# Performance work log

Hardware: AMD Instinct MI355X
Metric: run time of the kernel (lower is better)

Reference implementation:

```python
import jax, jax.numpy as jnp
import numpy as np

N_NODES = 100000
N_EDGES = 1600000
IN_F, OUT_F = 25, 50


def setup_inputs() -> dict:
    key = jax.random.key(0)
    k1, k2, k3, k4 = jax.random.split(key, 4)
    x = jax.random.normal(k1, (N_NODES, IN_F), dtype=jnp.float32)
    W = jax.random.normal(k2, (IN_F, OUT_F), dtype=jnp.float32) * (1.0 / np.sqrt(IN_F))
    b = jax.random.normal(k3, (OUT_F,), dtype=jnp.float32) * 0.01
    edge_index = jax.random.randint(k4, (2, N_EDGES), 0, N_NODES, dtype=jnp.int64)
    return {"x": x, "W": W, "b": b, "edge_index": edge_index}


def reference(x, W, b, edge_index):
    # GCNConv(normalize=False): linear transform, then add-aggregate over edges, + bias.
    src, dst = edge_index[0], edge_index[1]
    h = x @ W                                   # [N, OUT_F] small dense GEMM
    msgs = h[src]                               # [E, OUT_F] irregular gather
    agg = jax.ops.segment_sum(msgs, dst, num_segments=N_NODES)  # scatter-add to targets
    out = agg + b
    return jax.nn.relu(out)
```

## Files before the change

kernel.cpp:

```cpp
#include <hip/hip_runtime.h>

#define N_NODES 100000
#define N_EDGES 1600000
#define IN_F 25
#define OUT_F 50

#define BUCK_SHIFT 6
#define BUCK_NODES 64
#define NBUCK 1563
#define XW 16
#define SLAB 1280
#define BIN_NB 98
#define BIN_CHUNK 16384
#define XPREP_ITEMS (N_NODES * XW)
#define XPREP_NB 1563

__global__ __launch_bounds__(1024) void gcn_prep_kernel(
        const float* __restrict__ x,
        const int* __restrict__ ei,
        int* __restrict__ gfill,
        unsigned* __restrict__ recs,
        unsigned* __restrict__ xb) {
    __shared__ int lcnt[NBUCK];
    __shared__ int lbase[NBUCK];
    int tid = threadIdx.x, bid = blockIdx.x;
    if (bid < BIN_NB) {
        for (int i = tid; i < NBUCK; i += 1024) lcnt[i] = 0;
        __syncthreads();
        const int4* s4 = (const int4*)ei;
        const int4* d4 = (const int4*)(ei + N_EDGES);
        int base4 = bid * (BIN_CHUNK / 4);
        int4 sv[4], dv[4];
        bool ok[4];
#pragma unroll
        for (int k = 0; k < 4; ++k) {
            int i4 = base4 + k * 1024 + tid;
            ok[k] = (i4 < N_EDGES / 4);
            if (ok[k]) { dv[k] = d4[i4]; sv[k] = s4[i4]; }
        }
#pragma unroll
        for (int k = 0; k < 4; ++k) {
            if (ok[k]) {
                const int* dd = &dv[k].x;
#pragma unroll
                for (int c = 0; c < 4; ++c)
                    atomicAdd(&lcnt[((unsigned)dd[c]) >> BUCK_SHIFT], 1);
            }
        }
        __syncthreads();
        for (int i = tid; i < NBUCK; i += 1024) {
            int c = lcnt[i];
            lbase[i] = c ? atomicAdd(&gfill[i], c) : 0;
            lcnt[i] = 0;
        }
        __syncthreads();
#pragma unroll
        for (int k = 0; k < 4; ++k) {
            if (ok[k]) {
                const int* dd = &dv[k].x;
                const int* ss = &sv[k].x;
#pragma unroll
                for (int c = 0; c < 4; ++c) {
                    unsigned d = (unsigned)dd[c], s = (unsigned)ss[c];
                    int bk = d >> BUCK_SHIFT;
                    int p = lbase[bk] + atomicAdd(&lcnt[bk], 1);
                    if ((unsigned)p < SLAB)
                        recs[bk * SLAB + p] =
                            (s << BUCK_SHIFT) | (d & (BUCK_NODES - 1));
                }
            }
        }
    } else {
        int idx = (bid - BIN_NB) * 1024 + tid;
        if (idx >= XPREP_ITEMS) return;
        int n  = idx >> 4;
        int fp = (idx & 15) * 2;
        float v0 = (fp < IN_F) ? x[n * IN_F + fp] : 0.f;
        float v1 = (fp + 1 < IN_F) ? x[n * IN_F + fp + 1] : 0.f;
        union { float fl; unsigned u; } a, c;
        a.fl = v0; c.fl = v1;
        unsigned r0 = (a.u + 0x7FFFu + ((a.u >> 16) & 1u)) >> 16;
        unsigned r1 = (c.u + 0x7FFFu + ((c.u >> 16) & 1u)) >> 16;
        xb[idx] = (r1 << 16) | (r0 & 0xFFFFu);
    }
}

__global__ __launch_bounds__(512, 8) void gcn_k3_kernel(
        const uint2* __restrict__ xb2,
        const unsigned* __restrict__ recs,
        const int* __restrict__ gfill,
        const float* __restrict__ W,
        const float* __restrict__ b,
        float* __restrict__ out) {
    __shared__ unsigned raw[SLAB];
    __shared__ int      srt[SLAB];
    __shared__ int      cnt[BUCK_NODES], fil[BUCK_NODES], offs[BUCK_NODES + 1];
    __shared__ float    acc[BUCK_NODES * IN_F];
    __shared__ float    Ws[IN_F * OUT_F];
    __shared__ float    bs[OUT_F];

    int bk = blockIdx.x, tid = threadIdx.x;
    if (tid < BUCK_NODES) { cnt[tid] = 0; fil[tid] = 0; }
    for (int i = tid; i < IN_F * OUT_F; i += 512) Ws[i] = W[i];
    if (tid < OUT_F) bs[tid] = b[tid];
    __syncthreads();

    int cntE = min(gfill[bk], SLAB);
    const unsigned* rb = recs + bk * SLAB;

    for (int j = tid; j < cntE; j += 512) {
        unsigned rec = rb[j];
        raw[j] = rec;
        atomicAdd(&cnt[rec & (BUCK_NODES - 1)], 1);
    }
    __syncthreads();

    if (tid < 64) {
        int v = cnt[tid];
        for (int off = 1; off < 64; off <<= 1) {
            int t = __shfl_up(v, off, 64);
            if (tid >= off) v += t;
        }
        offs[tid + 1] = v;
        if (tid == 0) offs[0] = 0;
    }
    __syncthreads();

    for (int j = tid; j < cntE; j += 512) {
        unsigned rec = raw[j];
        int dl = rec & (BUCK_NODES - 1);
        int p = offs[dl] + atomicAdd(&fil[dl], 1);
        srt[p] = (int)(rec >> BUCK_SHIFT);
    }
    __syncthreads();

    {
        int g = tid >> 3, f = tid & 7;
        int e0 = offs[g], e1 = offs[g + 1];
        float a0 = 0.f, a1 = 0.f, a2 = 0.f, a3 = 0.f;
        int j = e0;
        for (; j + 8 <= e1; j += 8) {
            uint2 u[8];
#pragma unroll
            for (int q = 0; q < 8; ++q) u[q] = xb2[srt[j + q] * 8 + f];
#pragma unroll
            for (int q = 0; q < 8; ++q) {
                union { unsigned uu; float fl; } t0, t1, t2, t3;
                t0.uu = u[q].x << 16; t1.uu = u[q].x & 0xFFFF0000u;
                t2.uu = u[q].y << 16; t3.uu = u[q].y & 0xFFFF0000u;
                a0 += t0.fl; a1 += t1.fl; a2 += t2.fl; a3 += t3.fl;
            }
        }
        for (; j < e1; ++j) {
            uint2 u = xb2[srt[j] * 8 + f];
            union { unsigned uu; float fl; } t0, t1, t2, t3;
            t0.uu = u.x << 16; t1.uu = u.x & 0xFFFF0000u;
            t2.uu = u.y << 16; t3.uu = u.y & 0xFFFF0000u;
            a0 += t0.fl; a1 += t1.fl; a2 += t2.fl; a3 += t3.fl;
        }
        int ff = 4 * f;
        if (ff     < IN_F) acc[g * IN_F + ff]     = a0;
        if (ff + 1 < IN_F) acc[g * IN_F + ff + 1] = a1;
        if (ff + 2 < IN_F) acc[g * IN_F + ff + 2] = a2;
        if (ff + 3 < IN_F) acc[g * IN_F + ff + 3] = a3;
    }
    __syncthreads();

    int node0 = bk * BUCK_NODES;
    for (int i = tid; i < BUCK_NODES * OUT_F; i += 512) {
        int nl = i / OUT_F;
        int o  = i - nl * OUT_F;
        int node = node0 + nl;
        if (node < N_NODES) {
            float a = bs[o];
#pragma unroll
            for (int k = 0; k < IN_F; ++k)
                a += acc[nl * IN_F + k] * Ws[k * OUT_F + o];
            out[node * OUT_F + o] = fmaxf(a, 0.f);
        }
    }
}

extern "C" void kernel_launch(void* const* d_in, const int* in_sizes, int n_in,
                              void* d_out, int out_size, void* d_ws, size_t ws_size,
                              hipStream_t stream) {
    const float* x  = (const float*)d_in[0];
    const float* W  = (const float*)d_in[1];
    const float* b  = (const float*)d_in[2];
    const int*   ei = (const int*)d_in[3];
    float* out = (float*)d_out;

    char* ws = (char*)d_ws;
    unsigned* xb    = (unsigned*)(ws);
    unsigned* recs  = (unsigned*)(ws + 6400000);
    int*      gfill = (int*)(ws + 14402688);

    hipMemsetAsync(gfill, 0, NBUCK * sizeof(int), stream);
    gcn_prep_kernel<<<BIN_NB + XPREP_NB, 1024, 0, stream>>>(x, ei, gfill, recs, xb);
    gcn_k3_kernel<<<NBUCK, 512, 0, stream>>>((const uint2*)xb, recs, gfill, W, b, out);
}
```

Measured before the change: 138.1 us.

## Use 98-node buckets in 1024 blocks and grid-stride the x conversion

Buckets now hold 98 destination nodes instead of 64, so the aggregation kernel launches 1024 blocks (about four per CU) instead of 1563. Each block loops twice over its node groups, and the prefix scan is extended to cover 98 counters. The prep kernel's x-to-bf16 conversion now uses a grid-stride loop over a fixed 512-block grid, replacing one block per 1024 items. The intent is to cut tail effects and block launch overhead. The cost is integer division by 98 during binning, per-bucket slabs enlarged to 1920 records, and uneven thread use in the second group pass, since only 34 of 64 groups have nodes.

```diff
diff --git a/kernel.cpp b/kernel.cpp
--- a/kernel.cpp
+++ b/kernel.cpp
@@ -5,15 +5,14 @@
 #define IN_F 25
 #define OUT_F 50
 
-#define BUCK_SHIFT 6
-#define BUCK_NODES 64
-#define NBUCK 1563
-#define XW 16
-#define SLAB 1280
+#define BNODES 98
+#define NBUCK 1024
+#define DL_SHIFT 7
+#define SLAB 1920
 #define BIN_NB 98
 #define BIN_CHUNK 16384
-#define XPREP_ITEMS (N_NODES * XW)
-#define XPREP_NB 1563
+#define XPREP_ITEMS (N_NODES * 16)
+#define PREP_GRID 512
 
 __global__ __launch_bounds__(1024) void gcn_prep_kernel(
         const float* __restrict__ x,
@@ -44,7 +43,7 @@
                 const int* dd = &dv[k].x;
 #pragma unroll
                 for (int c = 0; c < 4; ++c)
-                    atomicAdd(&lcnt[((unsigned)dd[c]) >> BUCK_SHIFT], 1);
+                    atomicAdd(&lcnt[((unsigned)dd[c]) / BNODES], 1);
             }
         }
         __syncthreads();
@@ -62,26 +61,27 @@
 #pragma unroll
                 for (int c = 0; c < 4; ++c) {
                     unsigned d = (unsigned)dd[c], s = (unsigned)ss[c];
-                    int bk = d >> BUCK_SHIFT;
+                    unsigned bk = d / BNODES;
+                    unsigned dl = d - bk * BNODES;
                     int p = lbase[bk] + atomicAdd(&lcnt[bk], 1);
                     if ((unsigned)p < SLAB)
-                        recs[bk * SLAB + p] =
-                            (s << BUCK_SHIFT) | (d & (BUCK_NODES - 1));
+                        recs[bk * SLAB + p] = (s << DL_SHIFT) | dl;
                 }
             }
         }
     } else {
-        int idx = (bid - BIN_NB) * 1024 + tid;
-        if (idx >= XPREP_ITEMS) return;
-        int n  = idx >> 4;
-        int fp = (idx & 15) * 2;
-        float v0 = (fp < IN_F) ? x[n * IN_F + fp] : 0.f;
-        float v1 = (fp + 1 < IN_F) ? x[n * IN_F + fp + 1] : 0.f;
-        union { float fl; unsigned u; } a, c;
-        a.fl = v0; c.fl = v1;
-        unsigned r0 = (a.u + 0x7FFFu + ((a.u >> 16) & 1u)) >> 16;
-        unsigned r1 = (c.u + 0x7FFFu + ((c.u >> 16) & 1u)) >> 16;
-        xb[idx] = (r1 << 16) | (r0 & 0xFFFFu);
+        for (int idx = (bid - BIN_NB) * 1024 + tid; idx < XPREP_ITEMS;
+             idx += (PREP_GRID - BIN_NB) * 1024) {
+            int n  = idx >> 4;
+            int fp = (idx & 15) * 2;
+            float v0 = (fp < IN_F) ? x[n * IN_F + fp] : 0.f;
+            float v1 = (fp + 1 < IN_F) ? x[n * IN_F + fp + 1] : 0.f;
+            union { float fl; unsigned u; } a, c;
+            a.fl = v0; c.fl = v1;
+            unsigned r0 = (a.u + 0x7FFFu + ((a.u >> 16) & 1u)) >> 16;
+            unsigned r1 = (c.u + 0x7FFFu + ((c.u >> 16) & 1u)) >> 16;
+            xb[idx] = (r1 << 16) | (r0 & 0xFFFFu);
+        }
     }
 }
 
@@ -94,13 +94,14 @@
         float* __restrict__ out) {
     __shared__ unsigned raw[SLAB];
     __shared__ int      srt[SLAB];
-    __shared__ int      cnt[BUCK_NODES], fil[BUCK_NODES], offs[BUCK_NODES + 1];
-    __shared__ float    acc[BUCK_NODES * IN_F];
+    __shared__ int      cnt[128], fil[128];
+    __shared__ int      offs[BNODES + 1];
+    __shared__ float    acc[BNODES * IN_F];
     __shared__ float    Ws[IN_F * OUT_F];
     __shared__ float    bs[OUT_F];
 
     int bk = blockIdx.x, tid = threadIdx.x;
-    if (tid < BUCK_NODES) { cnt[tid] = 0; fil[tid] = 0; }
+    if (tid < 128) { cnt[tid] = 0; fil[tid] = 0; }
     for (int i = tid; i < IN_F * OUT_F; i += 512) Ws[i] = W[i];
     if (tid < OUT_F) bs[tid] = b[tid];
     __syncthreads();
@@ -111,7 +112,7 @@
     for (int j = tid; j < cntE; j += 512) {
         unsigned rec = rb[j];
         raw[j] = rec;
-        atomicAdd(&cnt[rec & (BUCK_NODES - 1)], 1);
+        atomicAdd(&cnt[rec & ((1 << DL_SHIFT) - 1)], 1);
     }
     __syncthreads();
 
@@ -122,52 +123,61 @@
             if (tid >= off) v += t;
         }
         offs[tid + 1] = v;
+        int t64 = __shfl(v, 63, 64);
+        int v2 = (tid < BNODES - 64) ? cnt[64 + tid] : 0;
+        for (int off = 1; off < 64; off <<= 1) {
+            int t = __shfl_up(v2, off, 64);
+            if (tid >= off) v2 += t;
+        }
+        if (tid < BNODES - 64) offs[65 + tid] = t64 + v2;
         if (tid == 0) offs[0] = 0;
     }
     __syncthreads();
 
     for (int j = tid; j < cntE; j += 512) {
         unsigned rec = raw[j];
-        int dl = rec & (BUCK_NODES - 1);
+        int dl = rec & ((1 << DL_SHIFT) - 1);
         int p = offs[dl] + atomicAdd(&fil[dl], 1);
-        srt[p] = (int)(rec >> BUCK_SHIFT);
+        srt[p] = (int)(rec >> DL_SHIFT);
     }
     __syncthreads();
 
     {
         int g = tid >> 3, f = tid & 7;
-        int e0 = offs[g], e1 = offs[g + 1];
-        float a0 = 0.f, a1 = 0.f, a2 = 0.f, a3 = 0.f;
-        int j = e0;
-        for (; j + 8 <= e1; j += 8) {
-            uint2 u[8];
-#pragma unroll
-            for (int q = 0; q < 8; ++q) u[q] = xb2[srt[j + q] * 8 + f];
-#pragma unroll
-            for (int q = 0; q < 8; ++q) {
+        for (int nl = g; nl < BNODES; nl += 64) {
+            int e0 = offs[nl], e1 = offs[nl + 1];
+            float a0 = 0.f, a1 = 0.f, a2 = 0.f, a3 = 0.f;
+            int j = e0;
+            for (; j + 8 <= e1; j += 8) {
+                uint2 u[8];
+#pragma unroll
+                for (int q = 0; q < 8; ++q) u[q] = xb2[srt[j + q] * 8 + f];
+#pragma unroll
+                for (int q = 0; q < 8; ++q) {
+                    union { unsigned uu; float fl; } t0, t1, t2, t3;
+                    t0.uu = u[q].x << 16; t1.uu = u[q].x & 0xFFFF0000u;
+                    t2.uu = u[q].y << 16; t3.uu = u[q].y & 0xFFFF0000u;
+                    a0 += t0.fl; a1 += t1.fl; a2 += t2.fl; a3 += t3.fl;
+                }
+            }
+            for (; j < e1; ++j) {
+                uint2 u = xb2[srt[j] * 8 + f];
                 union { unsigned uu; float fl; } t0, t1, t2, t3;
-                t0.uu = u[q].x << 16; t1.uu = u[q].x & 0xFFFF0000u;
-                t2.uu = u[q].y << 16; t3.uu = u[q].y & 0xFFFF0000u;
+                t0.uu = u.x << 16; t1.uu = u.x & 0xFFFF0000u;
+                t2.uu = u.y << 16; t3.uu = u.y & 0xFFFF0000u;
                 a0 += t0.fl; a1 += t1.fl; a2 += t2.fl; a3 += t3.fl;
             }
-        }
-        for (; j < e1; ++j) {
-            uint2 u = xb2[srt[j] * 8 + f];
-            union { unsigned uu; float fl; } t0, t1, t2, t3;
-            t0.uu = u.x << 16; t1.uu = u.x & 0xFFFF0000u;
-            t2.uu = u.y << 16; t3.uu = u.y & 0xFFFF0000u;
-            a0 += t0.fl; a1 += t1.fl; a2 += t2.fl; a3 += t3.fl;
-        }
-        int ff = 4 * f;
-        if (ff     < IN_F) acc[g * IN_F + ff]     = a0;
-        if (ff + 1 < IN_F) acc[g * IN_F + ff + 1] = a1;
-        if (ff + 2 < IN_F) acc[g * IN_F + ff + 2] = a2;
-        if (ff + 3 < IN_F) acc[g * IN_F + ff + 3] = a3;
-    }
-    __syncthreads();
-
-    int node0 = bk * BUCK_NODES;
-    for (int i = tid; i < BUCK_NODES * OUT_F; i += 512) {
+            int ff = 4 * f;
+            if (ff     < IN_F) acc[nl * IN_F + ff]     = a0;
+            if (ff + 1 < IN_F) acc[nl * IN_F + ff + 1] = a1;
+            if (ff + 2 < IN_F) acc[nl * IN_F + ff + 2] = a2;
+            if (ff + 3 < IN_F) acc[nl * IN_F + ff + 3] = a3;
+        }
+    }
+    __syncthreads();
+
+    int node0 = bk * BNODES;
+    for (int i = tid; i < BNODES * OUT_F; i += 512) {
         int nl = i / OUT_F;
         int o  = i - nl * OUT_F;
         int node = node0 + nl;
@@ -193,9 +203,9 @@
     char* ws = (char*)d_ws;
     unsigned* xb    = (unsigned*)(ws);
     unsigned* recs  = (unsigned*)(ws + 6400000);
-    int*      gfill = (int*)(ws + 14402688);
+    int*      gfill = (int*)(ws + 14264576);
 
     hipMemsetAsync(gfill, 0, NBUCK * sizeof(int), stream);
-    gcn_prep_kernel<<<BIN_NB + XPREP_NB, 1024, 0, stream>>>(x, ei, gfill, recs, xb);
+    gcn_prep_kernel<<<PREP_GRID, 1024, 0, stream>>>(x, ei, gfill, recs, xb);
     gcn_k3_kernel<<<NBUCK, 512, 0, stream>>>((const uint2*)xb, recs, gfill, W, b, out);
 }
```

Result: faster. 132.4 us (-4.1%).
